# Kernel optimization log

Measured on AMD Instinct MI355X. Metric: run time of the kernel, lower is better.

The kernel has to match this reference:

```python
import jax, jax.numpy as jnp
import numpy as np

B, N, C, H = 2, 2048, 768, 12
D = C // H  # head dim = 64


def _rotate_half(x):
    d2 = x.shape[-1] // 2
    x1, x2 = x[..., :d2], x[..., d2:]
    return jnp.concatenate([-x2, x1], axis=-1)


def _apply_rope(x, sin, cos):
    # x: [B,H,N,D], sin/cos: [N,D] -> broadcast over (B,H)
    return x * cos[None, None] + _rotate_half(x) * sin[None, None]


def setup_inputs() -> dict:
    key = jax.random.key(0)
    ks = jax.random.split(key, 7)
    x = jax.random.normal(ks[0], (B, N, C), dtype=jnp.float32)
    sin_spatial = jax.random.normal(ks[1], (N, D), dtype=jnp.float32)
    cos_spatial = jax.random.normal(ks[2], (N, D), dtype=jnp.float32)
    s = 1.0 / np.sqrt(C)
    W_qkv = jax.random.uniform(ks[3], (C, 3 * C), jnp.float32, -s, s)
    b_qkv = jax.random.uniform(ks[4], (3 * C,), jnp.float32, -s, s)
    W_out = jax.random.uniform(ks[5], (C, C), jnp.float32, -s, s)
    b_out = jax.random.uniform(ks[6], (C,), jnp.float32, -s, s)
    return {"x": x, "sin_spatial": sin_spatial, "cos_spatial": cos_spatial,
            "W_qkv": W_qkv, "b_qkv": b_qkv, "W_out": W_out, "b_out": b_out}


def reference(x, sin_spatial, cos_spatial, W_qkv, b_qkv, W_out, b_out):
    qkv = x @ W_qkv + b_qkv                       # [B,N,3C]
    qkv = qkv.reshape(B, N, 3, H, D).transpose(2, 0, 3, 1, 4)  # [3,B,H,N,D]
    q, k, v = qkv[0], qkv[1], qkv[2]
    q = _apply_rope(q, sin_spatial, cos_spatial)
    k = _apply_rope(k, sin_spatial, cos_spatial)
    att = jnp.einsum('bhqd,bhkd->bhqk', q, k) * (D ** -0.5)
    att = jax.nn.softmax(att, axis=-1)            # dropout is identity (eval)
    y = jnp.einsum('bhqk,bhkd->bhqd', att, v)     # [B,H,N,D]
    y = y.transpose(0, 2, 1, 3).reshape(B, N, C)
    return y @ W_out + b_out
```

## Files before the change

kernel.cpp:

```cpp
#include <hip/hip_runtime.h>
#include <hip/hip_bf16.h>

#define BB 2
#define NN 2048
#define CC 768
#define HH 12
#define DD 64
#define MM 4096
#define N3 2304

typedef __attribute__((ext_vector_type(8))) short bf16x8;
typedef __attribute__((ext_vector_type(4))) float f32x4;

#define QSCALE 0.18033688011112043f


__device__ __forceinline__ unsigned short f2bf(float f) {
    union { float f; unsigned u; } v; v.f = f;
    unsigned r = v.u + 0x7FFFu + ((v.u >> 16) & 1u);
    return (unsigned short)(r >> 16);
}

__device__ __forceinline__ short f2bf_rn(float f) {
    union { __hip_bfloat16 h; short s; } v;
    v.h = __float2bfloat16(f);
    return v.s;
}

__device__ __forceinline__ float exp2_hw(float x) {
    float r;
    asm("v_exp_f32 %0, %1" : "=v"(r) : "v"(x));
    return r;
}

__device__ __forceinline__ bf16x8 ld_frag16(const unsigned short* p) {
    bf16x8 r;
    __builtin_memcpy(&r, p, 16);
    return r;
}

__device__ __forceinline__ void gload16(const unsigned short* g, unsigned short* l) {
    __builtin_amdgcn_global_load_lds(
        (const __attribute__((address_space(1))) void*)g,
        (__attribute__((address_space(3))) void*)l,
        16, 0, 0);
}

__global__ void k_cvt(const float* __restrict__ s, unsigned short* __restrict__ d, int n4) {
    int i = blockIdx.x * blockDim.x + threadIdx.x;
    int st = gridDim.x * blockDim.x;
    for (; i < n4; i += st) {
        float4 v = ((const float4*)s)[i];
        ushort4 o;
        o.x = f2bf(v.x); o.y = f2bf(v.y); o.z = f2bf(v.z); o.w = f2bf(v.w);
        int f = i * 4;
        int dst = (f & ~31) + ((i & 3) << 3) + (((i >> 2) & 1) << 2);
        *(ushort4*)(d + dst) = o;
    }
}

__global__ void k_cvtT(const float* __restrict__ s, unsigned short* __restrict__ d,
                       int R, int Cc) {
    __shared__ unsigned short t[64][72];
    const int c0 = blockIdx.x * 64, r0 = blockIdx.y * 64;
    const int tr = threadIdx.x >> 4;
    const int tc = (threadIdx.x & 15) * 4;
#pragma unroll
    for (int i = 0; i < 4; i++) {
        int r = tr + i * 16;
        float4 v = *(const float4*)(s + (size_t)(r0 + r) * Cc + c0 + tc);
        t[tc + 0][r] = f2bf(v.x);
        t[tc + 1][r] = f2bf(v.y);
        t[tc + 2][r] = f2bf(v.z);
        t[tc + 3][r] = f2bf(v.w);
    }
    __syncthreads();
    const int wr = threadIdx.x >> 2;
    const int wc = (threadIdx.x & 3) * 16;
    unsigned short* drow = d + (size_t)(c0 + wr) * R + r0;
#pragma unroll
    for (int g = 0; g < 4; g++) {
        int k4 = wc + g * 4;
        int o = k4 & 31;
        int p = (((o & 15) >> 2) << 3) + (((o >> 4) & 1) << 2);
        ushort4 v4 = *(ushort4*)&t[wr][k4];
        *(ushort4*)(drow + (k4 & ~31) + p) = v4;
    }
}

__launch_bounds__(256)
__global__ void k_qkv(const unsigned short* __restrict__ xb,
                      const unsigned short* __restrict__ wt,
                      const float* __restrict__ bias,
                      const float* __restrict__ sinp,
                      const float* __restrict__ cosp,
                      unsigned short* __restrict__ qws,
                      unsigned short* __restrict__ kws,
                      unsigned short* __restrict__ vws) {
    __shared__ unsigned short As[2][128 * 32];
    __shared__ unsigned short Bs[2][64 * 32];
    const int tid = threadIdx.x;
    const int lane = tid & 63, w = tid >> 6;
    const int ql = lane & 15, lg = lane >> 4;
    const int row0 = blockIdx.x * 128;
    const int j0 = blockIdx.y * 64;

    f32x4 acc[2][4];
#pragma unroll
    for (int a = 0; a < 2; a++)
#pragma unroll
        for (int b = 0; b < 4; b++) acc[a][b] = f32x4{0.f, 0.f, 0.f, 0.f};

    const int sr = lane >> 2;
    const int sc = (lane & 3) * 8;

    auto stage = [&](int bi, int k0) {
#pragma unroll
        for (int c = 0; c < 2; c++) {
            int j = w * 2 + c;
            gload16(xb + (size_t)(row0 + j * 16 + sr) * CC + k0 + sc, &As[bi][j * 512]);
        }
        gload16(wt + (size_t)(j0 + w * 16 + sr) * CC + k0 + sc, &Bs[bi][w * 512]);
    };

    stage(0, 0);
    __syncthreads();

    int bufi = 0;
    for (int k0 = 0; k0 < CC; k0 += 32) {
        if (k0 + 32 < CC) stage(bufi ^ 1, k0 + 32);
        bf16x8 af[2], bfr[4];
#pragma unroll
        for (int fr = 0; fr < 2; fr++)
            af[fr] = ld_frag16(&As[bufi][(w * 32 + fr * 16 + ql) * 32 + lg * 8]);
#pragma unroll
        for (int fn = 0; fn < 4; fn++)
            bfr[fn] = ld_frag16(&Bs[bufi][(fn * 16 + ql) * 32 + lg * 8]);
#pragma unroll
        for (int fr = 0; fr < 2; fr++)
#pragma unroll
            for (int fn = 0; fn < 4; fn++)
                acc[fr][fn] = __builtin_amdgcn_mfma_f32_16x16x32_bf16(af[fr], bfr[fn], acc[fr][fn], 0, 0, 0);
        __syncthreads();
        bufi ^= 1;
    }

    float vals[2][4][4];
#pragma unroll
    for (int fr = 0; fr < 2; fr++)
#pragma unroll
        for (int fn = 0; fn < 4; fn++) {
            float bj = bias[j0 + fn * 16 + ql];
#pragma unroll
            for (int r = 0; r < 4; r++) vals[fr][fn][r] = acc[fr][fn][r] + bj;
        }
    const int t = j0 / CC;
    const int h = (j0 % CC) >> 6;
    if (t < 2) {
        unsigned short* outp = (t == 0) ? qws : kws;
        const float qs = (t == 0) ? QSCALE : 1.0f;
#pragma unroll
        for (int fr = 0; fr < 2; fr++)
#pragma unroll
            for (int r = 0; r < 4; r++) {
                int m = row0 + w * 32 + fr * 16 + lg * 4 + r;
                int b = m >> 11, n = m & (NN - 1);
#pragma unroll
                for (int fn = 0; fn < 4; fn++) {
                    int d = fn * 16 + ql;
                    float cv = cosp[n * DD + d], sv = sinp[n * DD + d];
                    float other = vals[fr][fn ^ 2][r];
                    float rv = (vals[fr][fn][r] * cv + ((fn < 2) ? -other : other) * sv) * qs;
                    int dcol = (fn >> 1) * 32 + (ql >> 2) * 8 + (fn & 1) * 4 + (ql & 3);
                    outp[((size_t)(b * HH + h) * NN + n) * DD + dcol] = f2bf(rv);
                }
            }
    } else {
#pragma unroll
        for (int fr = 0; fr < 2; fr++)
#pragma unroll
            for (int r = 0; r < 4; r++) {
                int m = row0 + w * 32 + fr * 16 + lg * 4 + r;
                int b = m >> 11, n = m & (NN - 1);
                int ncol = (n & ~31) + lg * 8 + (fr & 1) * 4 + r;
#pragma unroll
                for (int fn = 0; fn < 4; fn++) {
                    int d = fn * 16 + ql;
                    vws[((size_t)(b * HH + h) * DD + d) * NN + ncol] = f2bf(vals[fr][fn][r]);
                }
            }
    }
}

__launch_bounds__(128)
__global__ void k_attn(const unsigned short* __restrict__ qws,
                       const unsigned short* __restrict__ kws,
                       const unsigned short* __restrict__ vws,
                       unsigned short* __restrict__ yws) {
    __shared__ unsigned short Ks[2][64][72];
    __shared__ unsigned short Vs[2][64][72];
    const int tid = threadIdx.x;
    const int lane = tid & 63, w = tid >> 6;
    const int ql = lane & 15, lg = lane >> 4;
    const int d0 = blockIdx.x;
    const int bh = (d0 & 7) + 8 * (d0 >> 8);
    const int qb = (d0 >> 3) & 31;
    const int qw = qb * 64 + w * 32;
    const unsigned short* Qp = qws + (size_t)bh * NN * DD;
    const unsigned short* Kp = kws + (size_t)bh * NN * DD;
    const unsigned short* Vp = vws + (size_t)bh * DD * NN;

    bf16x8 qf[2][2];
#pragma unroll
    for (int fn = 0; fn < 2; fn++)
#pragma unroll
        for (int kb = 0; kb < 2; kb++)
            qf[fn][kb] = ld_frag16(Qp + (size_t)(qw + fn * 16 + ql) * DD + kb * 32 + lg * 8);

    f32x4 oacc[4][2];
#pragma unroll
    for (int a = 0; a < 4; a++)
#pragma unroll
        for (int b = 0; b < 2; b++) oacc[a][b] = f32x4{0.f, 0.f, 0.f, 0.f};
    float mrun[2] = {-1e30f, -1e30f}, lrun[2] = {0.f, 0.f};

    const int srow = tid >> 1;
    const int shalf = (tid & 1) * 32;

#pragma unroll
    for (int j = 0; j < 4; j++) {
        *(uint4*)&Ks[0][srow][shalf + j * 8] = *(const uint4*)(Kp + (size_t)srow * DD + shalf + j * 8);
        *(uint4*)&Vs[0][srow][shalf + j * 8] = *(const uint4*)(Vp + (size_t)srow * NN + shalf + j * 8);
    }
    __syncthreads();

    const int NT = NN / 64;
    int cur = 0;
    for (int kt = 0; kt < NT; kt++) {
        uint4 kn[4], vn[4];
        const bool hasn = (kt + 1 < NT);
        if (hasn) {
#pragma unroll
            for (int j = 0; j < 4; j++) {
                kn[j] = *(const uint4*)(Kp + (size_t)((kt + 1) * 64 + srow) * DD + shalf + j * 8);
                vn[j] = *(const uint4*)(Vp + (size_t)srow * NN + (kt + 1) * 64 + shalf + j * 8);
            }
        }
        const unsigned short (*Kc)[72] = Ks[cur];
        const unsigned short (*Vc)[72] = Vs[cur];

        f32x4 sacc[4][2];
#pragma unroll
        for (int a = 0; a < 4; a++)
#pragma unroll
            for (int b = 0; b < 2; b++) sacc[a][b] = f32x4{0.f, 0.f, 0.f, 0.f};
        __builtin_amdgcn_s_setprio(1);
#pragma unroll
        for (int kb = 0; kb < 2; kb++) {
            bf16x8 kf[4];
#pragma unroll
            for (int fr = 0; fr < 4; fr++)
                kf[fr] = ld_frag16(&Kc[fr * 16 + ql][kb * 32 + lg * 8]);
#pragma unroll
            for (int fr = 0; fr < 4; fr++)
#pragma unroll
                for (int fn = 0; fn < 2; fn++)
                    sacc[fr][fn] = __builtin_amdgcn_mfma_f32_16x16x32_bf16(kf[fr], qf[fn][kb], sacc[fr][fn], 0, 0, 0);
        }
        __builtin_amdgcn_s_setprio(0);

        bf16x8 pB[2][2];
#pragma unroll
        for (int fn = 0; fn < 2; fn++) {
            float ma = fmaxf(fmaxf(sacc[0][fn][0], sacc[0][fn][1]), fmaxf(sacc[0][fn][2], sacc[0][fn][3]));
            float mb = fmaxf(fmaxf(sacc[1][fn][0], sacc[1][fn][1]), fmaxf(sacc[1][fn][2], sacc[1][fn][3]));
            float mc = fmaxf(fmaxf(sacc[2][fn][0], sacc[2][fn][1]), fmaxf(sacc[2][fn][2], sacc[2][fn][3]));
            float md = fmaxf(fmaxf(sacc[3][fn][0], sacc[3][fn][1]), fmaxf(sacc[3][fn][2], sacc[3][fn][3]));
            float tm = fmaxf(fmaxf(ma, mb), fmaxf(mc, md));
            tm = fmaxf(tm, __shfl_xor(tm, 16));
            tm = fmaxf(tm, __shfl_xor(tm, 32));
            if (__any(tm > mrun[fn] + 8.0f)) {
                float mn = fmaxf(mrun[fn], tm);
                float scl = exp2_hw(mrun[fn] - mn);
                lrun[fn] *= scl;
#pragma unroll
                for (int db = 0; db < 4; db++) oacc[db][fn] *= scl;
                mrun[fn] = mn;
            }
            float ts = 0.f;
#pragma unroll
            for (int fr = 0; fr < 4; fr++)
#pragma unroll
                for (int r = 0; r < 4; r++) {
                    float p = exp2_hw(sacc[fr][fn][r] - mrun[fn]);
                    sacc[fr][fn][r] = p;
                    ts += p;
                }
            ts += __shfl_xor(ts, 16);
            ts += __shfl_xor(ts, 32);
            lrun[fn] += ts;

#pragma unroll
            for (int kkb = 0; kkb < 2; kkb++) {
                bf16x8 t8;
#pragma unroll
                for (int e = 0; e < 8; e++)
                    t8[e] = f2bf_rn(sacc[kkb * 2 + (e >> 2)][fn][e & 3]);
                pB[fn][kkb] = t8;
            }
        }

        __builtin_amdgcn_s_setprio(1);
#pragma unroll
        for (int db = 0; db < 4; db++) {
            bf16x8 va[2];
#pragma unroll
            for (int kkb = 0; kkb < 2; kkb++)
                va[kkb] = ld_frag16(&Vc[db * 16 + ql][kkb * 32 + lg * 8]);
#pragma unroll
            for (int kkb = 0; kkb < 2; kkb++)
#pragma unroll
                for (int fn = 0; fn < 2; fn++)
                    oacc[db][fn] = __builtin_amdgcn_mfma_f32_16x16x32_bf16(va[kkb], pB[fn][kkb], oacc[db][fn], 0, 0, 0);
        }
        __builtin_amdgcn_s_setprio(0);

        if (hasn) {
#pragma unroll
            for (int j = 0; j < 4; j++) {
                *(uint4*)&Ks[cur ^ 1][srow][shalf + j * 8] = kn[j];
                *(uint4*)&Vs[cur ^ 1][srow][shalf + j * 8] = vn[j];
            }
            __syncthreads();
            cur ^= 1;
        }
    }

    const int b = bh / HH, h = bh % HH;
#pragma unroll
    for (int fn = 0; fn < 2; fn++) {
        float inv = 1.0f / lrun[fn];
        int q = qw + fn * 16 + ql;
        unsigned short* yp = yws + (size_t)(b * NN + q) * CC + h * DD;
#pragma unroll
        for (int db = 0; db < 4; db++) {
            ushort4 o;
            o.x = f2bf(oacc[db][fn][0] * inv);
            o.y = f2bf(oacc[db][fn][1] * inv);
            o.z = f2bf(oacc[db][fn][2] * inv);
            o.w = f2bf(oacc[db][fn][3] * inv);
            *(ushort4*)(yp + (db >> 1) * 32 + lg * 8 + (db & 1) * 4) = o;
        }
    }
}

__launch_bounds__(256)
__global__ void k_out(const unsigned short* __restrict__ yb,
                      const unsigned short* __restrict__ wt,
                      const float* __restrict__ bias,
                      float* __restrict__ out) {
    __shared__ unsigned short As[2][128 * 32];
    __shared__ unsigned short Bs[2][64 * 32];
    const int tid = threadIdx.x;
    const int lane = tid & 63, w = tid >> 6;
    const int ql = lane & 15, lg = lane >> 4;
    const int row0 = blockIdx.x * 128;
    const int j0 = blockIdx.y * 64;

    f32x4 acc[2][4];
#pragma unroll
    for (int a = 0; a < 2; a++)
#pragma unroll
        for (int b = 0; b < 4; b++) acc[a][b] = f32x4{0.f, 0.f, 0.f, 0.f};

    const int sr = lane >> 2;
    const int sc = (lane & 3) * 8;

    auto stage = [&](int bi, int k0) {
#pragma unroll
        for (int c = 0; c < 2; c++) {
            int j = w * 2 + c;
            gload16(yb + (size_t)(row0 + j * 16 + sr) * CC + k0 + sc, &As[bi][j * 512]);
        }
        gload16(wt + (size_t)(j0 + w * 16 + sr) * CC + k0 + sc, &Bs[bi][w * 512]);
    };

    stage(0, 0);
    __syncthreads();

    int bufi = 0;
    for (int k0 = 0; k0 < CC; k0 += 32) {
        if (k0 + 32 < CC) stage(bufi ^ 1, k0 + 32);
        bf16x8 af[2], bfr[4];
#pragma unroll
        for (int fr = 0; fr < 2; fr++)
            af[fr] = ld_frag16(&As[bufi][(w * 32 + fr * 16 + ql) * 32 + lg * 8]);
#pragma unroll
        for (int fn = 0; fn < 4; fn++)
            bfr[fn] = ld_frag16(&Bs[bufi][(fn * 16 + ql) * 32 + lg * 8]);
#pragma unroll
        for (int fr = 0; fr < 2; fr++)
#pragma unroll
            for (int fn = 0; fn < 4; fn++)
                acc[fr][fn] = __builtin_amdgcn_mfma_f32_16x16x32_bf16(af[fr], bfr[fn], acc[fr][fn], 0, 0, 0);
        __syncthreads();
        bufi ^= 1;
    }

#pragma unroll
    for (int fr = 0; fr < 2; fr++)
#pragma unroll
        for (int fn = 0; fn < 4; fn++) {
            float bj = bias[j0 + fn * 16 + ql];
#pragma unroll
            for (int r = 0; r < 4; r++) {
                int m = row0 + w * 32 + fr * 16 + lg * 4 + r;
                out[(size_t)m * CC + j0 + fn * 16 + ql] = acc[fr][fn][r] + bj;
            }
        }
}

extern "C" void kernel_launch(void* const* d_in, const int* in_sizes, int n_in,
                              void* d_out, int out_size, void* d_ws, size_t ws_size,
                              hipStream_t stream) {
    const float* x    = (const float*)d_in[0];
    const float* sinp = (const float*)d_in[1];
    const float* cosp = (const float*)d_in[2];
    const float* wqkv = (const float*)d_in[3];
    const float* bqkv = (const float*)d_in[4];
    const float* wout = (const float*)d_in[5];
    const float* bout = (const float*)d_in[6];
    float* out = (float*)d_out;
    char* ws = (char*)d_ws;

    unsigned short* xb  = (unsigned short*)(ws);
    unsigned short* wqb = (unsigned short*)(ws + 6291456);
    unsigned short* wob = (unsigned short*)(ws + 9830400);
    unsigned short* qws = (unsigned short*)(ws + 11010048);
    unsigned short* kws = (unsigned short*)(ws + 17301504);
    unsigned short* vws = (unsigned short*)(ws + 23592960);
    unsigned short* yws = (unsigned short*)(ws + 29884416);
    if (ws_size < 36175872) return;

    k_cvt<<<dim3(512), dim3(256), 0, stream>>>(x, xb, MM * CC / 4);
    k_cvtT<<<dim3(36, 12), dim3(256), 0, stream>>>(wqkv, wqb, CC, N3);
    k_cvtT<<<dim3(12, 12), dim3(256), 0, stream>>>(wout, wob, CC, CC);
    k_qkv<<<dim3(32, 36), dim3(256), 0, stream>>>(xb, wqb, bqkv, sinp, cosp, qws, kws, vws);
    k_attn<<<dim3(768), dim3(128), 0, stream>>>(qws, kws, vws, yws);
    k_out<<<dim3(32, 12), dim3(256), 0, stream>>>(yws, wob, bout, out);
}
```

Before: 128.6 us.

## Split attention KV range in two and merge partials in combine kernel

Templates the attention kernel so each block can process half of the key/value sequence, doubling the grid from 768 to 1536 blocks. Per-half unnormalized outputs, running max and running sum are written to fp32 workspace, and a new combine kernel rescales and merges them into the bf16 output. This targets low occupancy on a device with many CUs, at the cost of extra global traffic for the partials (about 25MB), an extra launch, and a dependence on a larger workspace, falling back to the old path otherwise.

```diff
diff --git a/kernel.cpp b/kernel.cpp
--- a/kernel.cpp
+++ b/kernel.cpp
@@ -192,19 +192,31 @@
     }
 }
 
+template <int SPLITK>
 __launch_bounds__(128)
-__global__ void k_attn(const unsigned short* __restrict__ qws,
-                       const unsigned short* __restrict__ kws,
-                       const unsigned short* __restrict__ vws,
-                       unsigned short* __restrict__ yws) {
+__global__ void k_attn_t(const unsigned short* __restrict__ qws,
+                         const unsigned short* __restrict__ kws,
+                         const unsigned short* __restrict__ vws,
+                         unsigned short* __restrict__ yws,
+                         float* __restrict__ pA,
+                         float* __restrict__ pm,
+                         float* __restrict__ pl) {
     __shared__ unsigned short Ks[2][64][72];
     __shared__ unsigned short Vs[2][64][72];
     const int tid = threadIdx.x;
     const int lane = tid & 63, w = tid >> 6;
     const int ql = lane & 15, lg = lane >> 4;
     const int d0 = blockIdx.x;
-    const int bh = (d0 & 7) + 8 * (d0 >> 8);
-    const int qb = (d0 >> 3) & 31;
+    int bh, qb, kh;
+    if (SPLITK) {
+        bh = (d0 & 7) + 8 * (d0 >> 9);
+        qb = (d0 >> 3) & 31;
+        kh = (d0 >> 8) & 1;
+    } else {
+        bh = (d0 & 7) + 8 * (d0 >> 8);
+        qb = (d0 >> 3) & 31;
+        kh = 0;
+    }
     const int qw = qb * 64 + w * 32;
     const unsigned short* Qp = qws + (size_t)bh * NN * DD;
     const unsigned short* Kp = kws + (size_t)bh * NN * DD;
@@ -226,19 +238,21 @@
 
     const int srow = tid >> 1;
     const int shalf = (tid & 1) * 32;
+    const int kt0 = SPLITK ? kh * 16 : 0;
+    const int NT = SPLITK ? 16 : NN / 64;
 
 #pragma unroll
     for (int j = 0; j < 4; j++) {
-        *(uint4*)&Ks[0][srow][shalf + j * 8] = *(const uint4*)(Kp + (size_t)srow * DD + shalf + j * 8);
-        *(uint4*)&Vs[0][srow][shalf + j * 8] = *(const uint4*)(Vp + (size_t)srow * NN + shalf + j * 8);
+        *(uint4*)&Ks[0][srow][shalf + j * 8] = *(const uint4*)(Kp + (size_t)(kt0 * 64 + srow) * DD + shalf + j * 8);
+        *(uint4*)&Vs[0][srow][shalf + j * 8] = *(const uint4*)(Vp + (size_t)srow * NN + kt0 * 64 + shalf + j * 8);
     }
     __syncthreads();
 
-    const int NT = NN / 64;
     int cur = 0;
-    for (int kt = 0; kt < NT; kt++) {
+    for (int t = 0; t < NT; t++) {
+        const int kt = kt0 + t;
         uint4 kn[4], vn[4];
-        const bool hasn = (kt + 1 < NT);
+        const bool hasn = (t + 1 < NT);
         if (hasn) {
 #pragma unroll
             for (int j = 0; j < 4; j++) {
@@ -336,22 +350,63 @@
         }
     }
 
+    if (SPLITK) {
+#pragma unroll
+        for (int fn = 0; fn < 2; fn++) {
+            int q = qw + fn * 16 + ql;
+            float* ap = pA + (((size_t)kh * 24 + bh) * NN + q) * DD + lg * 4;
+#pragma unroll
+            for (int db = 0; db < 4; db++)
+                *(f32x4*)(ap + db * 16) = oacc[db][fn];
+            if (lg == 0) {
+                pm[((size_t)kh * 24 + bh) * NN + q] = mrun[fn];
+                pl[((size_t)kh * 24 + bh) * NN + q] = lrun[fn];
+            }
+        }
+    } else {
+        const int b = bh / HH, h = bh % HH;
+#pragma unroll
+        for (int fn = 0; fn < 2; fn++) {
+            float inv = 1.0f / lrun[fn];
+            int q = qw + fn * 16 + ql;
+            unsigned short* yp = yws + (size_t)(b * NN + q) * CC + h * DD;
+#pragma unroll
+            for (int db = 0; db < 4; db++) {
+                ushort4 o;
+                o.x = f2bf(oacc[db][fn][0] * inv);
+                o.y = f2bf(oacc[db][fn][1] * inv);
+                o.z = f2bf(oacc[db][fn][2] * inv);
+                o.w = f2bf(oacc[db][fn][3] * inv);
+                *(ushort4*)(yp + (db >> 1) * 32 + lg * 8 + (db & 1) * 4) = o;
+            }
+        }
+    }
+}
+
+__global__ void k_comb(const float* __restrict__ pA,
+                       const float* __restrict__ pm,
+                       const float* __restrict__ pl,
+                       unsigned short* __restrict__ yws) {
+    const int idx = blockIdx.x * blockDim.x + threadIdx.x;
+    const int qg = idx >> 4;
+    const int d4 = (idx & 15) * 4;
+    const int bh = qg >> 11, q = qg & (NN - 1);
     const int b = bh / HH, h = bh % HH;
-#pragma unroll
-    for (int fn = 0; fn < 2; fn++) {
-        float inv = 1.0f / lrun[fn];
-        int q = qw + fn * 16 + ql;
-        unsigned short* yp = yws + (size_t)(b * NN + q) * CC + h * DD;
-#pragma unroll
-        for (int db = 0; db < 4; db++) {
-            ushort4 o;
-            o.x = f2bf(oacc[db][fn][0] * inv);
-            o.y = f2bf(oacc[db][fn][1] * inv);
-            o.z = f2bf(oacc[db][fn][2] * inv);
-            o.w = f2bf(oacc[db][fn][3] * inv);
-            *(ushort4*)(yp + (db >> 1) * 32 + lg * 8 + (db & 1) * 4) = o;
-        }
-    }
+    const size_t half = (size_t)24 * NN * DD;
+    float m0 = pm[qg], m1 = pm[24 * NN + qg];
+    float l0 = pl[qg], l1 = pl[24 * NN + qg];
+    float M = fmaxf(m0, m1);
+    float e0 = exp2_hw(m0 - M), e1 = exp2_hw(m1 - M);
+    float inv = 1.0f / (l0 * e0 + l1 * e1);
+    f32x4 a0 = *(const f32x4*)(pA + (size_t)qg * DD + d4);
+    f32x4 a1 = *(const f32x4*)(pA + half + (size_t)qg * DD + d4);
+    ushort4 o;
+    o.x = f2bf((a0[0] * e0 + a1[0] * e1) * inv);
+    o.y = f2bf((a0[1] * e0 + a1[1] * e1) * inv);
+    o.z = f2bf((a0[2] * e0 + a1[2] * e1) * inv);
+    o.w = f2bf((a0[3] * e0 + a1[3] * e1) * inv);
+    int dcol = (d4 & ~31) + ((d4 >> 2) & 3) * 8 + ((d4 >> 4) & 1) * 4;
+    *(ushort4*)(yws + (size_t)(b * NN + q) * CC + h * DD + dcol) = o;
 }
 
 __launch_bounds__(256)
@@ -440,12 +495,21 @@
     unsigned short* kws = (unsigned short*)(ws + 17301504);
     unsigned short* vws = (unsigned short*)(ws + 23592960);
     unsigned short* yws = (unsigned short*)(ws + 29884416);
+    float* pA = (float*)(ws + 36175872);
+    float* pm = (float*)(ws + 61341696);
+    float* pl = (float*)(ws + 61734912);
     if (ws_size < 36175872) return;
+    const bool splitk = (ws_size >= 62128128);
 
     k_cvt<<<dim3(512), dim3(256), 0, stream>>>(x, xb, MM * CC / 4);
     k_cvtT<<<dim3(36, 12), dim3(256), 0, stream>>>(wqkv, wqb, CC, N3);
     k_cvtT<<<dim3(12, 12), dim3(256), 0, stream>>>(wout, wob, CC, CC);
     k_qkv<<<dim3(32, 36), dim3(256), 0, stream>>>(xb, wqb, bqkv, sinp, cosp, qws, kws, vws);
-    k_attn<<<dim3(768), dim3(128), 0, stream>>>(qws, kws, vws, yws);
+    if (splitk) {
+        k_attn_t<1><<<dim3(1536), dim3(128), 0, stream>>>(qws, kws, vws, yws, pA, pm, pl);
+        k_comb<<<dim3(3072), dim3(256), 0, stream>>>(pA, pm, pl, yws);
+    } else {
+        k_attn_t<0><<<dim3(768), dim3(128), 0, stream>>>(qws, kws, vws, yws, pA, pm, pl);
+    }
     k_out<<<dim3(32, 12), dim3(256), 0, stream>>>(yws, wob, bout, out);
 }
```

Result: slower. 137.6 us (+7.1%).
